# Performance work log

Hardware: AMD Instinct MI355X
Metric: run time of the kernel (lower is better)

## Reference

```python
import jax, jax.numpy as jnp
import numpy as np

TSZ, BSZ, E, H = 1024, 8, 1024, 16


def setup_inputs() -> dict:
    key = jax.random.key(0)
    ks = jax.random.split(key, 7)
    s = 0.02
    return {
        "q": jax.random.normal(ks[0], (TSZ, BSZ, E), jnp.float32),
        "k": jax.random.normal(ks[1], (TSZ, BSZ, E), jnp.float32),
        "v": jax.random.normal(ks[2], (TSZ, BSZ, E), jnp.float32),
        "in_proj_weight": jax.random.normal(ks[3], (3 * E, E), jnp.float32) * s,
        "in_proj_bias": jax.random.normal(ks[4], (3 * E,), jnp.float32) * s,
        "out_proj_weight": jax.random.normal(ks[5], (E, E), jnp.float32) * s,
        "out_proj_bias": jax.random.normal(ks[6], (E,), jnp.float32) * s,
        "num_heads": H,
    }


def reference(q, k, v, in_proj_weight, in_proj_bias, out_proj_weight, out_proj_bias, num_heads):
    tsz, bsz, embed_dim = q.shape
    head_dim = embed_dim // num_heads
    scaling = float(head_dim) ** -0.5

    # in-projections (F.linear: x @ W.T + b), weight sliced into q/k/v chunks
    qp = q @ in_proj_weight[:embed_dim].T + in_proj_bias[:embed_dim]
    kp = k @ in_proj_weight[embed_dim:2 * embed_dim].T + in_proj_bias[embed_dim:2 * embed_dim]
    vp = v @ in_proj_weight[2 * embed_dim:].T + in_proj_bias[2 * embed_dim:]
    qp = qp * scaling

    # (tsz, bsz, E) -> (bsz*H, tsz, head_dim)
    def to_heads(x):
        return x.reshape(tsz, bsz * num_heads, head_dim).transpose(1, 0, 2)

    qh, kh, vh = to_heads(qp), to_heads(kp), to_heads(vp)

    # scaled dot-product attention (no mask, dropout p=0)
    scores = jnp.einsum('bqd,bkd->bqk', qh, kh)  # [bsz*H, tsz, tsz]
    weights = jax.nn.softmax(scores, axis=-1)
    attn = jnp.einsum('bqk,bkd->bqd', weights, vh)

    # back to (tsz, bsz, E), then out projection
    attn = attn.transpose(1, 0, 2).reshape(tsz, bsz, embed_dim)
    out = attn @ out_proj_weight.T + out_proj_bias
    return out
```

## Files before the change

### kernel.cpp

```cpp
#include <hip/hip_runtime.h>

typedef __bf16 bf16;
typedef __attribute__((ext_vector_type(8))) __bf16 v8bf;
typedef __attribute__((ext_vector_type(4))) __bf16 v4bf;
typedef __attribute__((ext_vector_type(4))) float f32x4;

static_assert(sizeof(v8bf) == 16, "v8bf must be 16B");

#define MFMA16(a, b, c) __builtin_amdgcn_mfma_f32_16x16x32_bf16((a), (b), (c), 0, 0, 0)

__device__ __forceinline__ void async_lds16(const bf16* g, bf16* l) {
  __builtin_amdgcn_global_load_lds(
      (__attribute__((address_space(1))) void*)(g),
      (__attribute__((address_space(3))) void*)(l), 16, 0, 0);
}

__global__ __launch_bounds__(256) void cvt_kernel(
    const float* __restrict__ q, const float* __restrict__ k,
    const float* __restrict__ v, const float* __restrict__ wi,
    const float* __restrict__ wo, bf16* __restrict__ xq, bf16* __restrict__ xk,
    bf16* __restrict__ xv, bf16* __restrict__ Wb, bf16* __restrict__ Wob) {
  int idx = blockIdx.x * 256 + threadIdx.x;
  const float4* src;
  v4bf* dst;
  int off;
  if (idx < 2097152)      { src = (const float4*)q;  dst = (v4bf*)xq;  off = idx; }
  else if (idx < 4194304) { src = (const float4*)k;  dst = (v4bf*)xk;  off = idx - 2097152; }
  else if (idx < 6291456) { src = (const float4*)v;  dst = (v4bf*)xv;  off = idx - 4194304; }
  else if (idx < 7077888) { src = (const float4*)wi; dst = (v4bf*)Wb;  off = idx - 6291456; }
  else                    { src = (const float4*)wo; dst = (v4bf*)Wob; off = idx - 7077888; }
  float4 f = src[off];
  v4bf b;
  b[0] = (bf16)f.x; b[1] = (bf16)f.y; b[2] = (bf16)f.z; b[3] = (bf16)f.w;
  dst[off] = b;
}

#define TSZ 16384

#define STG_A(OB, CQ, KO)                                                     \
  async_lds16(Xa + (size_t)((CQ) * 65536 + (KO)) + srcoff,                    \
              Asmb + (OB) * TSZ + (CQ) * 4096 + dstW)
#define STG_B(OB, CQ, KO)                                                     \
  async_lds16(Wbase + (size_t)((CQ) * 65536 + (KO)) + srcoff,                 \
              Bsmb + (OB) * TSZ + (CQ) * 4096 + dstW)

#define WIN(BUF, OBUF, T)                                                     \
  do {                                                                        \
    const int t1 = (T) + 1, t2 = (T) + 2;                                     \
    const int ko1 = t1 * 64, ko2 = t2 * 64;                                   \
    v8bf a0[4], a1[4], bk0[4], bk1[4];                                        \
                                                             \
    _Pragma("unroll") for (int f = 0; f < 4; ++f)                             \
        a0[f] = *(const v8bf*)&Asmb[(BUF) * TSZ + aoff + f * 1024 + rs0];     \
    _Pragma("unroll") for (int nf = 0; nf < 4; ++nf)                          \
        bk0[nf] = *(const v8bf*)&Bsmb[(BUF) * TSZ + boff + nf * 1024 + rs0];  \
    if (t1 < 16) { STG_A(OBUF, 1, ko1); STG_A(OBUF, 3, ko1); }                \
    __builtin_amdgcn_s_barrier();                                             \
    __builtin_amdgcn_s_setprio(1);                                            \
    _Pragma("unroll") for (int f = 0; f < 4; ++f)                             \
        _Pragma("unroll") for (int nf = 0; nf < 4; ++nf)                      \
            acc[f][nf] = MFMA16(a0[f], bk0[nf], acc[f][nf]);                  \
    __builtin_amdgcn_s_setprio(0);                                            \
                                                             \
    _Pragma("unroll") for (int f = 0; f < 4; ++f)                             \
        a1[f] = *(const v8bf*)&Asmb[(BUF) * TSZ + aoff + f * 1024 + rs1];     \
    _Pragma("unroll") for (int nf = 0; nf < 4; ++nf)                          \
        bk1[nf] = *(const v8bf*)&Bsmb[(BUF) * TSZ + boff + nf * 1024 + rs1];  \
    if (t1 < 16) { STG_B(OBUF, 2, ko1); STG_B(OBUF, 3, ko1); }                \
    __builtin_amdgcn_s_barrier();                                             \
    __builtin_amdgcn_s_setprio(1);                                            \
    _Pragma("unroll") for (int f = 0; f < 4; ++f)                             \
        _Pragma("unroll") for (int nf = 0; nf < 4; ++nf)                      \
            acc[f][nf] = MFMA16(a1[f], bk1[nf], acc[f][nf]);                  \
    __builtin_amdgcn_s_setprio(0);                                            \
                                                             \
    _Pragma("unroll") for (int f = 0; f < 4; ++f)                             \
        a0[f] =                                                               \
            *(const v8bf*)&Asmb[(BUF) * TSZ + aoff + 4096 + f * 1024 + rs0];  \
    if (t2 < 16) { STG_A(BUF, 0, ko2); STG_A(BUF, 2, ko2); }                  \
    __builtin_amdgcn_s_barrier();                                             \
    __builtin_amdgcn_s_setprio(1);                                            \
    _Pragma("unroll") for (int f = 0; f < 4; ++f)                             \
        _Pragma("unroll") for (int nf = 0; nf < 4; ++nf)                      \
            acc[4 + f][nf] = MFMA16(a0[f], bk0[nf], acc[4 + f][nf]);          \
    __builtin_amdgcn_s_setprio(0);                                            \
                                                             \
    _Pragma("unroll") for (int f = 0; f < 4; ++f)                             \
        a1[f] =                                                               \
            *(const v8bf*)&Asmb[(BUF) * TSZ + aoff + 4096 + f * 1024 + rs1];  \
    if (t2 < 16) { STG_B(BUF, 0, ko2); STG_B(BUF, 1, ko2); }                  \
    if ((T) < 14) asm volatile("s_waitcnt vmcnt(4)" ::: "memory");            \
    else          asm volatile("s_waitcnt vmcnt(0)" ::: "memory");            \
    __builtin_amdgcn_s_barrier();                                             \
    __builtin_amdgcn_s_setprio(1);                                            \
    _Pragma("unroll") for (int f = 0; f < 4; ++f)                             \
        _Pragma("unroll") for (int nf = 0; nf < 4; ++nf)                      \
            acc[4 + f][nf] = MFMA16(a1[f], bk1[nf], acc[4 + f][nf]);          \
    __builtin_amdgcn_s_setprio(0);                                            \
  } while (0)

#define GEMM_PRELUDE()                                                        \
  const int tid = threadIdx.x;                                                \
  const int w = tid >> 6, l = tid & 63, quad = l >> 4, lr = l & 15;           \
  const int wmg = w >> 2, wng = w & 3;                                        \
  const int rbase = tid >> 3;                                                 \
  const int srcoff = rbase * 1024 + (((tid & 7) ^ (rbase & 7)) * 8);          \
  const int dstW = (tid & ~63) * 8;                                           \
  const int rs0 = ((quad) ^ (lr & 7)) * 8;                                    \
  const int rs1 = ((4 + quad) ^ (lr & 7)) * 8;                                \
  const int aoff = (wmg * 128 + lr) * 64;                                     \
  const int boff = (wng * 64 + lr) * 64;                                      \
  f32x4 acc[8][4] = {};                                                       \
   \
  _Pragma("unroll") for (int cq = 0; cq < 4; ++cq) {                          \
    STG_A(0, cq, 0);                                                          \
    STG_B(0, cq, 0);                                                          \
  }                                                                           \
  STG_A(1, 0, 64);                                                            \
  STG_A(1, 2, 64);                                                            \
  STG_B(1, 0, 64);                                                            \
  STG_B(1, 1, 64);                                                            \
  asm volatile("s_waitcnt vmcnt(4)" ::: "memory");                            \
  __builtin_amdgcn_s_barrier();                                               \
  _Pragma("unroll 1") for (int ip = 0; ip < 8; ++ip) {                        \
    WIN(0, 1, 2 * ip);                                                        \
    WIN(1, 0, 2 * ip + 1);                                                    \
  }

__global__ __launch_bounds__(512, 2) void qkv_proj_kernel(
    const bf16* __restrict__ xq, const bf16* __restrict__ xk,
    const bf16* __restrict__ xv, const bf16* __restrict__ Wb,
    const float* __restrict__ bias, bf16* __restrict__ oq,
    bf16* __restrict__ ok, bf16* __restrict__ ov) {
  __shared__ bf16 Asm2[2][TSZ];
  __shared__ bf16 Bsm2[2][TSZ];
  bf16* Asmb = &Asm2[0][0];
  bf16* Bsmb = &Bsm2[0][0];
  const int L = blockIdx.x;
  const int g = L >> 5;
  const int c = g >> 2;
  const int n0 = (g & 3) * 256;
  const int m0 = (L & 31) * 256;
  const bf16* X = (c == 0) ? xq : (c == 1) ? xk : xv;
  bf16* outp = (c == 0) ? oq : (c == 1) ? ok : ov;
  const bf16* Xa = X + (size_t)m0 * 1024;
  const bf16* Wbase = Wb + ((size_t)(c * 1024 + n0)) * 1024;

  GEMM_PRELUDE();

  const float scale = (c == 0) ? 0.125f : 1.0f;
#pragma unroll
  for (int mf = 0; mf < 8; ++mf)
#pragma unroll
    for (int nf = 0; nf < 4; ++nf) {
      const int n = n0 + wng * 64 + nf * 16 + lr;
      const float bn = bias[c * 1024 + n];
      const int hh = n >> 6, d = n & 63;
#pragma unroll
      for (int j = 0; j < 4; ++j) {
        const int m = m0 + wmg * 128 + (mf >> 2) * 64 + (mf & 3) * 16 +
                      quad * 4 + j;
        const int t_ = m >> 3, b = m & 7;
        outp[((size_t)((b * 16 + hh) * 1024 + t_)) * 64 + d] =
            (bf16)((acc[mf][nf][j] + bn) * scale);
      }
    }
}

__global__ __launch_bounds__(256) void transpose_v_kernel(const bf16* __restrict__ vin,
                                                          bf16* __restrict__ vout) {
  __shared__ bf16 tile[64][72];
  const int bh = blockIdx.x;
  const int t0 = blockIdx.y * 64;
  const int tid = threadIdx.x;
  const int row = tid >> 2, cg = (tid & 3) * 16;
  const bf16* src = vin + ((size_t)bh * 1024 + t0 + row) * 64 + cg;
#pragma unroll
  for (int i = 0; i < 2; ++i) {
    v8bf x = *(const v8bf*)(src + i * 8);
#pragma unroll
    for (int jj = 0; jj < 8; ++jj) tile[row][cg + i * 8 + jj] = x[jj];
  }
  __syncthreads();
  const int d = tid >> 2, tg = (tid & 3) * 16;
  bf16* dst = vout + ((size_t)bh * 64 + d) * 1024 + t0 + tg;
  v8bf o0, o1;
#pragma unroll
  for (int i = 0; i < 8; ++i) o0[i] = tile[tg + i][d];
#pragma unroll
  for (int i = 0; i < 8; ++i) o1[i] = tile[tg + 8 + i][d];
  *(v8bf*)dst = o0;
  *(v8bf*)(dst + 8) = o1;
}

#define KSTR 72
#define VSTR 136

__global__ __launch_bounds__(256, 2) void attn_kernel(const bf16* __restrict__ qh,
                                                      const bf16* __restrict__ kh,
                                                      const bf16* __restrict__ vT,
                                                      bf16* __restrict__ attn_out) {
  __shared__ bf16 Ksm[128 * KSTR];
  __shared__ bf16 Vsm[64 * VSTR];
  __shared__ bf16 Psm[128 * VSTR];
  const int L = blockIdx.x;
  const int bh = (L & 7) * 16 + ((L >> 3) & 15);
  const int t0 = (L >> 7) * 128;
  const int tid = threadIdx.x;
  const int w = tid >> 6, l = tid & 63, quad = l >> 4, lr = l & 15;
  const int qr0 = t0 + w * 32;

  const bf16* khead = kh + (size_t)bh * 1024 * 64;
  const bf16* vhead = vT + (size_t)bh * 64 * 1024;

  const size_t qbase = ((size_t)bh * 1024 + qr0 + lr) * 64 + quad * 8;
  const v8bf bq00 = *(const v8bf*)(qh + qbase);
  const v8bf bq01 = *(const v8bf*)(qh + qbase + 32);
  const v8bf bq10 = *(const v8bf*)(qh + qbase + 1024);
  const v8bf bq11 = *(const v8bf*)(qh + qbase + 1024 + 32);

  const int krow = tid >> 1, kd = (tid & 1) * 32;
  const int vrow = tid >> 2, vk = (tid & 3) * 32;
  const bf16* kg = khead + (size_t)krow * 64 + kd;
  const bf16* vg = vhead + (size_t)vrow * 1024 + vk;
  bf16* Kw = &Ksm[krow * KSTR + kd];
  bf16* Vw = &Vsm[vrow * VSTR + vk];
  bf16* Pw = &Psm[w * 32 * VSTR];

  v8bf kst[4], vst[4];
#pragma unroll
  for (int i = 0; i < 4; ++i) kst[i] = *(const v8bf*)(kg + i * 8);
#pragma unroll
  for (int i = 0; i < 4; ++i) vst[i] = *(const v8bf*)(vg + i * 8);

  float rsum0 = 0.0f, rsum1 = 0.0f;
  f32x4 oacc0[4] = {}, oacc1[4] = {};

  for (int c = 0; c < 8; ++c) {
    __syncthreads();
#pragma unroll
    for (int i = 0; i < 4; ++i) *(v8bf*)(Kw + i * 8) = kst[i];
#pragma unroll
    for (int i = 0; i < 4; ++i) *(v8bf*)(Vw + i * 8) = vst[i];
    __syncthreads();
    if (c < 7) {
      const bf16* kg2 = kg + (size_t)(c + 1) * 128 * 64;
      const bf16* vg2 = vg + (c + 1) * 128;
#pragma unroll
      for (int i = 0; i < 4; ++i) kst[i] = *(const v8bf*)(kg2 + i * 8);
#pragma unroll
      for (int i = 0; i < 4; ++i) vst[i] = *(const v8bf*)(vg2 + i * 8);
    }

#pragma unroll
    for (int kt = 0; kt < 8; ++kt) {
      const v8bf ak0 = *(const v8bf*)&Ksm[(kt * 16 + lr) * KSTR + quad * 8];
      const v8bf ak1 = *(const v8bf*)&Ksm[(kt * 16 + lr) * KSTR + 32 + quad * 8];
      f32x4 a = {};
      a = MFMA16(ak0, bq00, a);
      a = MFMA16(ak1, bq01, a);
      f32x4 b = {};
      b = MFMA16(ak0, bq10, b);
      b = MFMA16(ak1, bq11, b);
      v4bf pb0, pb1;
#pragma unroll
      for (int j = 0; j < 4; ++j) {
        const float p0 = __expf(a[j]);
        const float p1 = __expf(b[j]);
        rsum0 += p0;
        rsum1 += p1;
        pb0[j] = (bf16)p0;
        pb1[j] = (bf16)p1;
      }
      *(v4bf*)(Pw + lr * VSTR + kt * 16 + quad * 4) = pb0;
      *(v4bf*)(Pw + (16 + lr) * VSTR + kt * 16 + quad * 4) = pb1;
    }

#pragma unroll
    for (int ks = 0; ks < 4; ++ks) {
      const v8bf pa0 = *(const v8bf*)(Pw + lr * VSTR + ks * 32 + quad * 8);
      const v8bf pa1 = *(const v8bf*)(Pw + (16 + lr) * VSTR + ks * 32 + quad * 8);
#pragma unroll
      for (int dt = 0; dt < 4; ++dt) {
        const v8bf vb = *(const v8bf*)&Vsm[(dt * 16 + lr) * VSTR + ks * 32 + quad * 8];
        oacc0[dt] = MFMA16(pa0, vb, oacc0[dt]);
        oacc1[dt] = MFMA16(pa1, vb, oacc1[dt]);
      }
    }
  }

  rsum0 += __shfl_xor(rsum0, 16);
  rsum0 += __shfl_xor(rsum0, 32);
  rsum1 += __shfl_xor(rsum1, 16);
  rsum1 += __shfl_xor(rsum1, 32);
  const float inv0 = 1.0f / rsum0;
  const float inv1 = 1.0f / rsum1;
  const int b = bh >> 4, h = bh & 15;
#pragma unroll
  for (int j = 0; j < 4; ++j) {
    const float i0 = __shfl(inv0, quad * 4 + j);
    const float i1 = __shfl(inv1, quad * 4 + j);
    const int t0j = qr0 + quad * 4 + j;
#pragma unroll
    for (int dt = 0; dt < 4; ++dt) {
      attn_out[((size_t)(t0j * 8 + b)) * 1024 + h * 64 + dt * 16 + lr] =
          (bf16)(oacc0[dt][j] * i0);
      attn_out[((size_t)((t0j + 16) * 8 + b)) * 1024 + h * 64 + dt * 16 + lr] =
          (bf16)(oacc1[dt][j] * i1);
    }
  }
}

__global__ __launch_bounds__(512, 2) void out_proj_kernel(const bf16* __restrict__ A,
                                                          const bf16* __restrict__ Wob,
                                                          const float* __restrict__ bias,
                                                          float* __restrict__ out) {
  __shared__ bf16 Asm2[2][TSZ];
  __shared__ bf16 Bsm2[2][TSZ];
  bf16* Asmb = &Asm2[0][0];
  bf16* Bsmb = &Bsm2[0][0];
  const int L = blockIdx.x;
  const int n0 = (L >> 5) * 256;
  const int m0 = (L & 31) * 256;
  const bf16* Xa = A + (size_t)m0 * 1024;
  const bf16* Wbase = Wob + (size_t)n0 * 1024;

  GEMM_PRELUDE();

#pragma unroll
  for (int mf = 0; mf < 8; ++mf)
#pragma unroll
    for (int nf = 0; nf < 4; ++nf) {
      const int n = n0 + wng * 64 + nf * 16 + lr;
      const float bn = bias[n];
#pragma unroll
      for (int j = 0; j < 4; ++j) {
        const int m = m0 + wmg * 128 + (mf >> 2) * 64 + (mf & 3) * 16 +
                      quad * 4 + j;
        out[(size_t)m * 1024 + n] = acc[mf][nf][j] + bn;
      }
    }
}

extern "C" void kernel_launch(void* const* d_in, const int* in_sizes, int n_in,
                              void* d_out, int out_size, void* d_ws, size_t ws_size,
                              hipStream_t stream) {
  const float* q  = (const float*)d_in[0];
  const float* k  = (const float*)d_in[1];
  const float* v  = (const float*)d_in[2];
  const float* wi = (const float*)d_in[3];
  const float* bi = (const float*)d_in[4];
  const float* wo = (const float*)d_in[5];
  const float* bo = (const float*)d_in[6];
  float* out = (float*)d_out;
  char* ws = (char*)d_ws;
  const size_t MB = (size_t)1 << 20;
  bf16* Wb     = (bf16*)(ws + 0 * MB);
  bf16* Wob    = (bf16*)(ws + 6 * MB);
  bf16* wsq    = (bf16*)(ws + 8 * MB);
  bf16* wsk    = (bf16*)(ws + 24 * MB);
  bf16* wsv    = (bf16*)(ws + 40 * MB);
  bf16* xv     = (bf16*)(ws + 56 * MB);
  bf16* wsvT   = (bf16*)(ws + 56 * MB);
  bf16* xq     = (bf16*)d_out;
  bf16* xk     = (bf16*)((char*)d_out + 16 * MB);
  bf16* wsattn = wsv;

  cvt_kernel<<<dim3(28672), dim3(256), 0, stream>>>(q, k, v, wi, wo, xq, xk, xv, Wb, Wob);
  qkv_proj_kernel<<<dim3(384), dim3(512), 0, stream>>>(xq, xk, xv, Wb, bi, wsq, wsk, wsv);
  transpose_v_kernel<<<dim3(128, 16), dim3(256), 0, stream>>>(wsv, wsvT);
  attn_kernel<<<dim3(1024), dim3(256), 0, stream>>>(wsq, wsk, wsvT, wsattn);
  out_proj_kernel<<<dim3(128), dim3(512), 0, stream>>>(wsattn, Wob, bo, out);
}
```

Before: 299.6 us.

## Retile projection GEMMs to 256x128 tiles with 3-stage A / 2-stage B pipeline

Both projection GEMM kernels drop from 512-thread 256x256 tiles with a K-step of 64 and double-buffered LDS to 256-thread 256x128 tiles with a K-step of 32. A is triple-buffered and B double-buffered, and the LDS swizzle is adjusted to the narrower rows. Grids double (768 and 256 blocks) to raise block count and occupancy, out_proj in particular going from 128 to 256 blocks. The cost is lower arithmetic intensity per tile and more barriers per unit of K.

```diff
diff --git a/kernel.cpp b/kernel.cpp
--- a/kernel.cpp
+++ b/kernel.cpp
@@ -35,111 +35,94 @@
   dst[off] = b;
 }
 
-#define TSZ 16384
-
-#define STG_A(OB, CQ, KO)                                                     \
-  async_lds16(Xa + (size_t)((CQ) * 65536 + (KO)) + srcoff,                    \
-              Asmb + (OB) * TSZ + (CQ) * 4096 + dstW)
-#define STG_B(OB, CQ, KO)                                                     \
-  async_lds16(Wbase + (size_t)((CQ) * 65536 + (KO)) + srcoff,                 \
-              Bsmb + (OB) * TSZ + (CQ) * 4096 + dstW)
-
-#define WIN(BUF, OBUF, T)                                                     \
+#define AB2_(AB) (((AB) + 2) % 3)
+
+#define STG_A4(AB, KO)                                                        \
   do {                                                                        \
-    const int t1 = (T) + 1, t2 = (T) + 2;                                     \
-    const int ko1 = t1 * 64, ko2 = t2 * 64;                                   \
-    v8bf a0[4], a1[4], bk0[4], bk1[4];                                        \
-                                                             \
-    _Pragma("unroll") for (int f = 0; f < 4; ++f)                             \
-        a0[f] = *(const v8bf*)&Asmb[(BUF) * TSZ + aoff + f * 1024 + rs0];     \
-    _Pragma("unroll") for (int nf = 0; nf < 4; ++nf)                          \
-        bk0[nf] = *(const v8bf*)&Bsmb[(BUF) * TSZ + boff + nf * 1024 + rs0];  \
-    if (t1 < 16) { STG_A(OBUF, 1, ko1); STG_A(OBUF, 3, ko1); }                \
+    _Pragma("unroll") for (int cc = 0; cc < 4; ++cc)                          \
+        async_lds16(Xa + (size_t)cc * 65536 + srcoff + (KO),                  \
+                    Asmb + (AB) * 8192 + cc * 2048 + wdst);                   \
+  } while (0)
+
+#define STG_B2(BB, KO)                                                        \
+  do {                                                                        \
+    _Pragma("unroll") for (int cc = 0; cc < 2; ++cc)                          \
+        async_lds16(Wbase + (size_t)cc * 65536 + srcoff + (KO),               \
+                    Bsmb + (BB) * 4096 + cc * 2048 + wdst);                   \
+  } while (0)
+
+#define RD_A(AB, G)                                                           \
+  _Pragma("unroll") for (int f = 0; f < 4; ++f)                               \
+      ar[f] = *(const v8bf*)&Asmb[(AB) * 8192 + arow + (G) * 2048 +           \
+                                  f * 512 + slot8];
+
+#define RD_B(BB)                                                              \
+  _Pragma("unroll") for (int nf = 0; nf < 4; ++nf)                            \
+      br[nf] = *(const v8bf*)&Bsmb[(BB) * 4096 + brow + nf * 512 + slot8];
+
+#define MM(OFF)                                                               \
+  __builtin_amdgcn_s_setprio(1);                                              \
+  _Pragma("unroll") for (int f = 0; f < 4; ++f)                               \
+      _Pragma("unroll") for (int nf = 0; nf < 4; ++nf)                        \
+          acc[(OFF) + f][nf] = MFMA16(ar[f], br[nf], acc[(OFF) + f][nf]);     \
+  __builtin_amdgcn_s_setprio(0);
+
+#define STEP(T, AB, BB, SB, SA, VM)                                           \
+  do {                                                                        \
+    v8bf ar[4], br[4];                                                        \
+    RD_A(AB, 0);                                                              \
+    RD_B(BB);                                                                 \
+    if (SB) STG_B2((BB) ^ 1, ((T) + 1) * 32);                                 \
     __builtin_amdgcn_s_barrier();                                             \
-    __builtin_amdgcn_s_setprio(1);                                            \
-    _Pragma("unroll") for (int f = 0; f < 4; ++f)                             \
-        _Pragma("unroll") for (int nf = 0; nf < 4; ++nf)                      \
-            acc[f][nf] = MFMA16(a0[f], bk0[nf], acc[f][nf]);                  \
-    __builtin_amdgcn_s_setprio(0);                                            \
-                                                             \
-    _Pragma("unroll") for (int f = 0; f < 4; ++f)                             \
-        a1[f] = *(const v8bf*)&Asmb[(BUF) * TSZ + aoff + f * 1024 + rs1];     \
-    _Pragma("unroll") for (int nf = 0; nf < 4; ++nf)                          \
-        bk1[nf] = *(const v8bf*)&Bsmb[(BUF) * TSZ + boff + nf * 1024 + rs1];  \
-    if (t1 < 16) { STG_B(OBUF, 2, ko1); STG_B(OBUF, 3, ko1); }                \
+    MM(0);                                                                    \
+    RD_A(AB, 1);                                                              \
+    if (SA) STG_A4(AB2_(AB), ((T) + 2) * 32);                                 \
+    if ((VM) == 4) { asm volatile("s_waitcnt vmcnt(4)" ::: "memory"); }       \
+    else if ((VM) == 0) { asm volatile("s_waitcnt vmcnt(0)" ::: "memory"); }  \
     __builtin_amdgcn_s_barrier();                                             \
-    __builtin_amdgcn_s_setprio(1);                                            \
-    _Pragma("unroll") for (int f = 0; f < 4; ++f)                             \
-        _Pragma("unroll") for (int nf = 0; nf < 4; ++nf)                      \
-            acc[f][nf] = MFMA16(a1[f], bk1[nf], acc[f][nf]);                  \
-    __builtin_amdgcn_s_setprio(0);                                            \
-                                                             \
-    _Pragma("unroll") for (int f = 0; f < 4; ++f)                             \
-        a0[f] =                                                               \
-            *(const v8bf*)&Asmb[(BUF) * TSZ + aoff + 4096 + f * 1024 + rs0];  \
-    if (t2 < 16) { STG_A(BUF, 0, ko2); STG_A(BUF, 2, ko2); }                  \
-    __builtin_amdgcn_s_barrier();                                             \
-    __builtin_amdgcn_s_setprio(1);                                            \
-    _Pragma("unroll") for (int f = 0; f < 4; ++f)                             \
-        _Pragma("unroll") for (int nf = 0; nf < 4; ++nf)                      \
-            acc[4 + f][nf] = MFMA16(a0[f], bk0[nf], acc[4 + f][nf]);          \
-    __builtin_amdgcn_s_setprio(0);                                            \
-                                                             \
-    _Pragma("unroll") for (int f = 0; f < 4; ++f)                             \
-        a1[f] =                                                               \
-            *(const v8bf*)&Asmb[(BUF) * TSZ + aoff + 4096 + f * 1024 + rs1];  \
-    if (t2 < 16) { STG_B(BUF, 0, ko2); STG_B(BUF, 1, ko2); }                  \
-    if ((T) < 14) asm volatile("s_waitcnt vmcnt(4)" ::: "memory");            \
-    else          asm volatile("s_waitcnt vmcnt(0)" ::: "memory");            \
-    __builtin_amdgcn_s_barrier();                                             \
-    __builtin_amdgcn_s_setprio(1);                                            \
-    _Pragma("unroll") for (int f = 0; f < 4; ++f)                             \
-        _Pragma("unroll") for (int nf = 0; nf < 4; ++nf)                      \
-            acc[4 + f][nf] = MFMA16(a1[f], bk1[nf], acc[4 + f][nf]);          \
-    __builtin_amdgcn_s_setprio(0);                                            \
+    MM(4);                                                                    \
   } while (0)
 
 #define GEMM_PRELUDE()                                                        \
   const int tid = threadIdx.x;                                                \
   const int w = tid >> 6, l = tid & 63, quad = l >> 4, lr = l & 15;           \
-  const int wmg = w >> 2, wng = w & 3;                                        \
-  const int rbase = tid >> 3;                                                 \
-  const int srcoff = rbase * 1024 + (((tid & 7) ^ (rbase & 7)) * 8);          \
-  const int dstW = (tid & ~63) * 8;                                           \
-  const int rs0 = ((quad) ^ (lr & 7)) * 8;                                    \
-  const int rs1 = ((4 + quad) ^ (lr & 7)) * 8;                                \
-  const int aoff = (wmg * 128 + lr) * 64;                                     \
-  const int boff = (wng * 64 + lr) * 64;                                      \
+  const int wmg = w >> 1, wng = w & 1;                                        \
+  const int slot8 = (quad ^ ((lr >> 1) & 3)) * 8;                             \
+  const int arow = (wmg * 128 + lr) * 32;                                     \
+  const int brow = (wng * 64 + lr) * 32;                                      \
+  const int wdst = (tid & ~63) * 8;                                           \
+  const int srow = tid >> 2;                                                  \
+  const int srcoff = srow * 1024 + (((tid & 3) ^ ((srow >> 1) & 3)) * 8);     \
   f32x4 acc[8][4] = {};                                                       \
-   \
-  _Pragma("unroll") for (int cq = 0; cq < 4; ++cq) {                          \
-    STG_A(0, cq, 0);                                                          \
-    STG_B(0, cq, 0);                                                          \
-  }                                                                           \
-  STG_A(1, 0, 64);                                                            \
-  STG_A(1, 2, 64);                                                            \
-  STG_B(1, 0, 64);                                                            \
-  STG_B(1, 1, 64);                                                            \
+  STG_A4(0, 0);                                                               \
+  STG_B2(0, 0);                                                               \
+  STG_A4(1, 32);                                                              \
   asm volatile("s_waitcnt vmcnt(4)" ::: "memory");                            \
   __builtin_amdgcn_s_barrier();                                               \
-  _Pragma("unroll 1") for (int ip = 0; ip < 8; ++ip) {                        \
-    WIN(0, 1, 2 * ip);                                                        \
-    WIN(1, 0, 2 * ip + 1);                                                    \
-  }
-
-__global__ __launch_bounds__(512, 2) void qkv_proj_kernel(
+  _Pragma("unroll 1") for (int tt = 0; tt < 30; tt += 6) {                    \
+    STEP(tt + 0, 0, 0, 1, 1, 4);                                              \
+    STEP(tt + 1, 1, 1, 1, 1, 4);                                              \
+    STEP(tt + 2, 2, 0, 1, 1, 4);                                              \
+    STEP(tt + 3, 0, 1, 1, 1, 4);                                              \
+    STEP(tt + 4, 1, 0, 1, 1, 4);                                              \
+    STEP(tt + 5, 2, 1, 1, 1, 4);                                              \
+  }                                                                           \
+  STEP(30, 0, 0, 1, 0, 0);                                                    \
+  STEP(31, 1, 1, 0, 0, -1);
+
+__global__ __launch_bounds__(256, 2) void qkv_proj_kernel(
     const bf16* __restrict__ xq, const bf16* __restrict__ xk,
     const bf16* __restrict__ xv, const bf16* __restrict__ Wb,
     const float* __restrict__ bias, bf16* __restrict__ oq,
     bf16* __restrict__ ok, bf16* __restrict__ ov) {
-  __shared__ bf16 Asm2[2][TSZ];
-  __shared__ bf16 Bsm2[2][TSZ];
-  bf16* Asmb = &Asm2[0][0];
-  bf16* Bsmb = &Bsm2[0][0];
+  __shared__ bf16 Asm3[3][8192];
+  __shared__ bf16 Bsm3[2][4096];
+  bf16* Asmb = &Asm3[0][0];
+  bf16* Bsmb = &Bsm3[0][0];
   const int L = blockIdx.x;
   const int g = L >> 5;
-  const int c = g >> 2;
-  const int n0 = (g & 3) * 256;
+  const int c = g >> 3;
+  const int n0 = (g & 7) * 128;
   const int m0 = (L & 31) * 256;
   const bf16* X = (c == 0) ? xq : (c == 1) ? xk : xv;
   bf16* outp = (c == 0) ? oq : (c == 1) ? ok : ov;
@@ -311,16 +294,16 @@
   }
 }
 
-__global__ __launch_bounds__(512, 2) void out_proj_kernel(const bf16* __restrict__ A,
+__global__ __launch_bounds__(256, 2) void out_proj_kernel(const bf16* __restrict__ A,
                                                           const bf16* __restrict__ Wob,
                                                           const float* __restrict__ bias,
                                                           float* __restrict__ out) {
-  __shared__ bf16 Asm2[2][TSZ];
-  __shared__ bf16 Bsm2[2][TSZ];
-  bf16* Asmb = &Asm2[0][0];
-  bf16* Bsmb = &Bsm2[0][0];
+  __shared__ bf16 Asm3[3][8192];
+  __shared__ bf16 Bsm3[2][4096];
+  bf16* Asmb = &Asm3[0][0];
+  bf16* Bsmb = &Bsm3[0][0];
   const int L = blockIdx.x;
-  const int n0 = (L >> 5) * 256;
+  const int n0 = (L >> 5) * 128;
   const int m0 = (L & 31) * 256;
   const bf16* Xa = A + (size_t)m0 * 1024;
   const bf16* Wbase = Wob + (size_t)n0 * 1024;
@@ -367,8 +350,8 @@
   bf16* wsattn = wsv;
 
   cvt_kernel<<<dim3(28672), dim3(256), 0, stream>>>(q, k, v, wi, wo, xq, xk, xv, Wb, Wob);
-  qkv_proj_kernel<<<dim3(384), dim3(512), 0, stream>>>(xq, xk, xv, Wb, bi, wsq, wsk, wsv);
+  qkv_proj_kernel<<<dim3(768), dim3(256), 0, stream>>>(xq, xk, xv, Wb, bi, wsq, wsk, wsv);
   transpose_v_kernel<<<dim3(128, 16), dim3(256), 0, stream>>>(wsv, wsvT);
   attn_kernel<<<dim3(1024), dim3(256), 0, stream>>>(wsq, wsk, wsvT, wsattn);
-  out_proj_kernel<<<dim3(128), dim3(512), 0, stream>>>(wsattn, Wob, bo, out);
-}
+  out_proj_kernel<<<dim3(256), dim3(256), 0, stream>>>(wsattn, Wob, bo, out);
+}
```

After: 300.7 us. Within noise of the previous version (+0.4%).
